# Kernel tuning notes

Hardware: AMD Instinct MI355X
Metric: run time of the kernel (lower is better)

## Reference

```python
import jax, jax.numpy as jnp
import numpy as np

N_NODES = 50000
N_EDGES = 800000
IN_C, HID_C, OUT_C = 256, 256, 128


def setup_inputs() -> dict:
    key = jax.random.key(0)
    k1, k2, k3, k4 = jax.random.split(key, 4)
    x = jax.random.normal(k1, (N_NODES, IN_C), dtype=jnp.float32)
    edge_index = jax.random.randint(k2, (2, N_EDGES), 0, N_NODES, dtype=jnp.int64)
    # Glorot-ish init for linear weights, zero bias (PyG GCNConv default)
    W1 = jax.random.normal(k3, (IN_C, HID_C), dtype=jnp.float32) / np.sqrt(IN_C)
    b1 = jnp.zeros((HID_C,), dtype=jnp.float32)
    W2 = jax.random.normal(k4, (HID_C, OUT_C), dtype=jnp.float32) / np.sqrt(HID_C)
    b2 = jnp.zeros((OUT_C,), dtype=jnp.float32)
    return {"x": x, "edge_index": edge_index, "W1": W1, "b1": b1, "W2": W2, "b2": b2}


def _gcn_conv(x, src, dst, norm, W, b):
    # Linear transform first (dense GEMM), then normalized scatter-add aggregation.
    h = x @ W                                   # [N, out]
    msg = h[src] * norm[:, None]                # [E+N, out] gathered, scaled messages
    out = jax.ops.segment_sum(msg, dst, num_segments=x.shape[0])
    return out + b


def reference(x, edge_index, W1, b1, W2, b2):
    n = x.shape[0]
    loops = jnp.arange(n, dtype=edge_index.dtype)
    # PyG GCNConv: add self-loops, symmetric normalization D^-1/2 A D^-1/2
    src = jnp.concatenate([edge_index[0], loops])
    dst = jnp.concatenate([edge_index[1], loops])
    deg = jnp.zeros((n,), dtype=x.dtype).at[dst].add(1.0)
    dinv = jnp.where(deg > 0, jax.lax.rsqrt(deg), 0.0)
    norm = dinv[src] * dinv[dst]                # [E+N]
    h = jax.nn.relu(_gcn_conv(x, src, dst, norm, W1, b1))
    return _gcn_conv(h, src, dst, norm, W2, b2)
```

## Files before the change

kernel.cpp:

```cpp
#include <hip/hip_runtime.h>


#define NN 50000
#define EE 800000
#define IN_C 256
#define HID_C 256
#define OUT_C 128
#define CAP 64
#define FILLB 2048

typedef __attribute__((ext_vector_type(8))) short short8;
typedef __attribute__((ext_vector_type(4))) float f32x4;
typedef __attribute__((ext_vector_type(2))) float f32x2;

static __device__ __forceinline__ ushort f2b(float f) {
    union { float f; unsigned u; } v; v.f = f;
    unsigned r = v.u + 0x7FFF + ((v.u >> 16) & 1);
    return (ushort)(r >> 16);
}


__global__ __launch_bounds__(256) void build_kernel(
    const int* __restrict__ src, const int* __restrict__ dst,
    int* __restrict__ cnt, ushort* __restrict__ slots,
    ushort* __restrict__ hb, ushort* __restrict__ h2b, int e) {
    const int bid = blockIdx.x;
    const int tid = threadIdx.x;
    if (bid < FILLB) {
        const int xcd = bid & 7;
        const int lo = xcd * (NN / 8);
        const int hi = lo + (NN / 8);
        const int sub = bid >> 3;
        for (int i = sub * 256 + tid; i < e; i += 256 * 256) {
            int d = dst[i];
            if (d >= lo && d < hi) {
                int s = src[i];
                int pos = atomicAdd(&cnt[d], 1);
                if (pos < CAP) slots[(size_t)d * CAP + pos] = (ushort)s;
            }
        }
    } else {
        ushort4 z = {0, 0, 0, 0};
        if (tid < 64) ((ushort4*)(hb + (size_t)NN * HID_C))[tid] = z;
        else if (tid < 96) ((ushort4*)(h2b + (size_t)NN * OUT_C))[tid - 64] = z;
    }
}


template <bool A_FP32, int NHALF>
__global__ __launch_bounds__(256) void gemm_kernel(
    const void* __restrict__ Av, const float* __restrict__ W,
    const int* __restrict__ cnt, ushort* __restrict__ C, int M, int Ntot) {
    constexpr int KK = 256;
    __shared__ ushort wt[128 * KK];

    const int tid = threadIdx.x;
    const int rowBase = blockIdx.x * 128;

    const int wave = tid >> 6, lane = tid & 63;
    const int l15 = lane & 15, lk = lane >> 4;

    int r0 = rowBase + wave * 32 + l15;
    int ra0 = min(r0, M - 1);
    int ra1 = min(r0 + 16, M - 1);

    short8 a0f[8], a1f[8];
    if constexpr (A_FP32) {
        const float* A = (const float*)Av;
        const float* Ar0 = A + (size_t)ra0 * KK + lk * 8;
        const float* Ar1 = A + (size_t)ra1 * KK + lk * 8;
#pragma unroll
        for (int ks = 0; ks < 8; ++ks) {
            float4 p0 = *(const float4*)(Ar0 + ks * 32);
            float4 p1 = *(const float4*)(Ar0 + ks * 32 + 4);
            float4 q0 = *(const float4*)(Ar1 + ks * 32);
            float4 q1 = *(const float4*)(Ar1 + ks * 32 + 4);
            short8 a, b;
            a[0] = f2b(p0.x); a[1] = f2b(p0.y); a[2] = f2b(p0.z); a[3] = f2b(p0.w);
            a[4] = f2b(p1.x); a[5] = f2b(p1.y); a[6] = f2b(p1.z); a[7] = f2b(p1.w);
            b[0] = f2b(q0.x); b[1] = f2b(q0.y); b[2] = f2b(q0.z); b[3] = f2b(q0.w);
            b[4] = f2b(q1.x); b[5] = f2b(q1.y); b[6] = f2b(q1.z); b[7] = f2b(q1.w);
            a0f[ks] = a; a1f[ks] = b;
        }
    } else {
        const ushort* A = (const ushort*)Av;
        const ushort* Ar0 = A + (size_t)ra0 * KK + lk * 8;
        const ushort* Ar1 = A + (size_t)ra1 * KK + lk * 8;
#pragma unroll
        for (int ks = 0; ks < 8; ++ks) {
            a0f[ks] = *(const short8*)(Ar0 + ks * 32);
            a1f[ks] = *(const short8*)(Ar1 + ks * 32);
        }
    }

    for (int hh = 0; hh < NHALF; ++hh) {
        const int colBase = hh * 128;
        for (int it = 0; it < 32; ++it) {
            int item = tid + it * 256;
            int n = item & 127;
            int kg = item >> 7;
            int k = kg * 4;
            const float* wp = W + (size_t)k * Ntot + colBase + n;
            ushort4 o;
            o.x = f2b(wp[0]);
            o.y = f2b(wp[Ntot]);
            o.z = f2b(wp[2 * Ntot]);
            o.w = f2b(wp[3 * Ntot]);
            *(ushort4*)((char*)wt + n * 512 + ((kg * 8) ^ ((n & 7) << 4))) = o;
        }
        __syncthreads();

        f32x4 acc[2][8] = {};
#pragma unroll
        for (int ks = 0; ks < 8; ++ks) {
            int kbyte = ks * 64 + lk * 16;
#pragma unroll
            for (int nt = 0; nt < 8; ++nt) {
                int n = nt * 16 + l15;
                short8 b = *(const short8*)((const char*)wt + n * 512 + (kbyte ^ ((n & 7) << 4)));
                acc[0][nt] = __builtin_amdgcn_mfma_f32_16x16x32_bf16(a0f[ks], b, acc[0][nt], 0, 0, 0);
                acc[1][nt] = __builtin_amdgcn_mfma_f32_16x16x32_bf16(a1f[ks], b, acc[1][nt], 0, 0, 0);
            }
        }

#pragma unroll
        for (int t = 0; t < 2; ++t) {
            int rbase = rowBase + wave * 32 + t * 16 + lk * 4;
#pragma unroll
            for (int r = 0; r < 4; ++r) {
                int row = rbase + r;
                if (row < M) {
                    float dv = rsqrtf((float)(cnt[row] + 1));
#pragma unroll
                    for (int nt = 0; nt < 8; ++nt)
                        C[(size_t)row * Ntot + colBase + nt * 16 + l15] = f2b(acc[t][nt][r] * dv);
                }
            }
        }
        if (hh + 1 < NHALF) __syncthreads();
    }
}


template <int C, bool RELU, bool OUT_BF16>
__global__ __launch_bounds__(256) void gather_kernel(
    const ushort* __restrict__ h, const int* __restrict__ cnt,
    const ushort* __restrict__ slots, const float* __restrict__ bias,
    void* __restrict__ out, int n) {
    constexpr int VPL = C / 64;
    const int node = blockIdx.x * 4 + (threadIdx.x >> 6);
    if (node >= n) return;
    const int lane = threadIdx.x & 63;
    const int c0 = cnt[node];
    const int deg = min(c0, CAP);
    const ushort* sl = slots + (size_t)node * CAP;
    const ushort* hl = h + lane * VPL;

    f32x2 acc01 = {0.f, 0.f}, acc23 = {0.f, 0.f};

    auto addu = [&](unsigned u, f32x2& acc) {
        f32x2 p;
        p.x = __uint_as_float(u << 16);
        p.y = __uint_as_float(u & 0xFFFF0000u);
        acc += p;
    };

    for (int base = 0; base < deg; base += 16) {
        uint4 pa = *(const uint4*)(sl + base);
        uint4 pb = *(const uint4*)(sl + base + 8);
        int id[16];
        id[0]  = pa.x & 0xFFFF; id[1]  = pa.x >> 16;
        id[2]  = pa.y & 0xFFFF; id[3]  = pa.y >> 16;
        id[4]  = pa.z & 0xFFFF; id[5]  = pa.z >> 16;
        id[6]  = pa.w & 0xFFFF; id[7]  = pa.w >> 16;
        id[8]  = pb.x & 0xFFFF; id[9]  = pb.x >> 16;
        id[10] = pb.y & 0xFFFF; id[11] = pb.y >> 16;
        id[12] = pb.z & 0xFFFF; id[13] = pb.z >> 16;
        id[14] = pb.w & 0xFFFF; id[15] = pb.w >> 16;
        int ix[16];
#pragma unroll
        for (int j = 0; j < 16; ++j) ix[j] = (base + j < deg) ? id[j] : n;
        if constexpr (VPL == 4) {
            uint2 v[16];
#pragma unroll
            for (int j = 0; j < 16; ++j) v[j] = *(const uint2*)(hl + (size_t)ix[j] * C);
#pragma unroll
            for (int j = 0; j < 16; ++j) { addu(v[j].x, acc01); addu(v[j].y, acc23); }
        } else {
            unsigned v[16];
#pragma unroll
            for (int j = 0; j < 16; ++j) v[j] = *(const unsigned*)(hl + (size_t)ix[j] * C);
#pragma unroll
            for (int j = 0; j < 16; ++j) addu(v[j], acc01);
        }
    }

    if constexpr (VPL == 4) {
        uint2 v = *(const uint2*)(hl + (size_t)node * C);
        addu(v.x, acc01); addu(v.y, acc23);
    } else {
        unsigned v = *(const unsigned*)(hl + (size_t)node * C);
        addu(v, acc01);
    }

    const float dv = rsqrtf((float)(c0 + 1));
    const float* bp = bias + lane * VPL;
    float r[VPL];
    r[0] = acc01.x * dv + bp[0];
    r[1] = acc01.y * dv + bp[1];
    if constexpr (VPL == 4) {
        r[2] = acc23.x * dv + bp[2];
        r[3] = acc23.y * dv + bp[3];
    }
#pragma unroll
    for (int k = 0; k < VPL; ++k)
        if (RELU) r[k] = fmaxf(r[k], 0.0f);

    if constexpr (OUT_BF16) {
        ushort* op = (ushort*)out + (size_t)node * C + lane * VPL;
#pragma unroll
        for (int k = 0; k < VPL; ++k) op[k] = f2b(r[k]);
    } else {
        float* op = (float*)out + (size_t)node * C + lane * VPL;
#pragma unroll
        for (int k = 0; k < VPL; ++k) op[k] = r[k];
    }
}


extern "C" void kernel_launch(void* const* d_in, const int* in_sizes, int n_in,
                              void* d_out, int out_size, void* d_ws, size_t ws_size,
                              hipStream_t stream) {
    const float* x  = (const float*)d_in[0];
    const int*   ei = (const int*)d_in[1];
    const float* W1 = (const float*)d_in[2];
    const float* b1 = (const float*)d_in[3];
    const float* W2 = (const float*)d_in[4];
    const float* b2 = (const float*)d_in[5];
    float* out = (float*)d_out;

    const int N = in_sizes[0] / IN_C;
    const int E = in_sizes[1] / 2;
    const int* src = ei;
    const int* dst = ei + E;

    char* ws = (char*)d_ws;
    int*    cnt   = (int*)(ws + (256 << 10));
    ushort* slots = (ushort*)(ws + (512 << 10));
    ushort* hb    = (ushort*)(ws + (size_t)(40 << 20));
    ushort* h1b   = (ushort*)(ws + (size_t)(66 << 20));
    ushort* h2b   = (ushort*)(ws + (size_t)(92 << 20));

    hipMemsetAsync(cnt, 0, (size_t)N * sizeof(int), stream);
    build_kernel<<<FILLB + 1, 256, 0, stream>>>(src, dst, cnt, slots, hb, h2b, E);

    gemm_kernel<true, 2><<<(N + 127) / 128, 256, 0, stream>>>(x, W1, cnt, hb, N, HID_C);
    gather_kernel<HID_C, true, true><<<(N + 3) / 4, 256, 0, stream>>>(
        hb, cnt, slots, b1, h1b, N);

    gemm_kernel<false, 1><<<(N + 127) / 128, 256, 0, stream>>>(h1b, W2, cnt, h2b, N, OUT_C);
    gather_kernel<OUT_C, false, false><<<(N + 3) / 4, 256, 0, stream>>>(
        h2b, cnt, slots, b2, out, N);
}
```

Measured before the change: 183.8 us.

## Fuse first GEMM with CSR build and weight layer-1 gather by source dinv

Merges the adjacency-building kernel and the first GEMM into one launch, so the GEMM blocks run alongside the atomic slot fill instead of waiting for it. Because the GEMM no longer knows the degrees, the source-side normalisation moves into the layer-1 gather as a per-neighbour dinv weight, and a small dinv kernel precomputes rsqrt degrees. Counters are split into two halves per node to reduce atomic contention. The cost is an extra launch, an extra dinv gather per neighbour in layer 1, and two segment loops per node.

New measurement: 248.9 us. 1.35x slower.

```diff
diff --git a/kernel.cpp b/kernel.cpp
--- a/kernel.cpp
+++ b/kernel.cpp
@@ -7,7 +7,9 @@
 #define HID_C 256
 #define OUT_C 128
 #define CAP 64
+#define SEGC 32
 #define FILLB 2048
+#define G1B 391
 
 typedef __attribute__((ext_vector_type(8))) short short8;
 typedef __attribute__((ext_vector_type(4))) float f32x4;
@@ -20,43 +22,43 @@
 }
 
 
-__global__ __launch_bounds__(256) void build_kernel(
+__global__ __launch_bounds__(256) void fused1_kernel(
+    const float* __restrict__ x, const float* __restrict__ W1,
     const int* __restrict__ src, const int* __restrict__ dst,
     int* __restrict__ cnt, ushort* __restrict__ slots,
-    ushort* __restrict__ hb, ushort* __restrict__ h2b, int e) {
+    ushort* __restrict__ hb, ushort* __restrict__ h2b, int e, int M) {
     const int bid = blockIdx.x;
     const int tid = threadIdx.x;
-    if (bid < FILLB) {
-        const int xcd = bid & 7;
-        const int lo = xcd * (NN / 8);
-        const int hi = lo + (NN / 8);
-        const int sub = bid >> 3;
-        for (int i = sub * 256 + tid; i < e; i += 256 * 256) {
-            int d = dst[i];
-            if (d >= lo && d < hi) {
-                int s = src[i];
-                int pos = atomicAdd(&cnt[d], 1);
-                if (pos < CAP) slots[(size_t)d * CAP + pos] = (ushort)s;
-            }
-        }
-    } else {
-        ushort4 z = {0, 0, 0, 0};
-        if (tid < 64) ((ushort4*)(hb + (size_t)NN * HID_C))[tid] = z;
-        else if (tid < 96) ((ushort4*)(h2b + (size_t)NN * OUT_C))[tid - 64] = z;
-    }
-}
-
-
-template <bool A_FP32, int NHALF>
-__global__ __launch_bounds__(256) void gemm_kernel(
-    const void* __restrict__ Av, const float* __restrict__ W,
-    const int* __restrict__ cnt, ushort* __restrict__ C, int M, int Ntot) {
+
+    if (bid >= G1B) {
+        if (bid < G1B + FILLB) {
+            const int fb = bid - G1B;
+            const int xcd = fb & 7;
+            const int lo = xcd * (NN / 8);
+            const int hi = lo + (NN / 8);
+            const int sub = fb >> 3;
+            const int half = sub >> 7;
+            for (int i = sub * 256 + tid; i < e; i += 256 * 256) {
+                int d = dst[i];
+                if (d >= lo && d < hi) {
+                    int s = src[i];
+                    int pos = atomicAdd(&cnt[2 * d + half], 1);
+                    if (pos < SEGC)
+                        slots[(size_t)d * CAP + half * SEGC + pos] = (ushort)s;
+                }
+            }
+        } else {
+            ushort4 z = {0, 0, 0, 0};
+            if (tid < 64) ((ushort4*)(hb + (size_t)NN * HID_C))[tid] = z;
+            else if (tid < 96) ((ushort4*)(h2b + (size_t)NN * OUT_C))[tid - 64] = z;
+        }
+        return;
+    }
+
     constexpr int KK = 256;
     __shared__ ushort wt[128 * KK];
 
-    const int tid = threadIdx.x;
-    const int rowBase = blockIdx.x * 128;
-
+    const int rowBase = bid * 128;
     const int wave = tid >> 6, lane = tid & 63;
     const int l15 = lane & 15, lk = lane >> 4;
 
@@ -65,10 +67,9 @@
     int ra1 = min(r0 + 16, M - 1);
 
     short8 a0f[8], a1f[8];
-    if constexpr (A_FP32) {
-        const float* A = (const float*)Av;
-        const float* Ar0 = A + (size_t)ra0 * KK + lk * 8;
-        const float* Ar1 = A + (size_t)ra1 * KK + lk * 8;
+    {
+        const float* Ar0 = x + (size_t)ra0 * KK + lk * 8;
+        const float* Ar1 = x + (size_t)ra1 * KK + lk * 8;
 #pragma unroll
         for (int ks = 0; ks < 8; ++ks) {
             float4 p0 = *(const float4*)(Ar0 + ks * 32);
@@ -82,30 +83,21 @@
             b[4] = f2b(q1.x); b[5] = f2b(q1.y); b[6] = f2b(q1.z); b[7] = f2b(q1.w);
             a0f[ks] = a; a1f[ks] = b;
         }
-    } else {
-        const ushort* A = (const ushort*)Av;
-        const ushort* Ar0 = A + (size_t)ra0 * KK + lk * 8;
-        const ushort* Ar1 = A + (size_t)ra1 * KK + lk * 8;
-#pragma unroll
-        for (int ks = 0; ks < 8; ++ks) {
-            a0f[ks] = *(const short8*)(Ar0 + ks * 32);
-            a1f[ks] = *(const short8*)(Ar1 + ks * 32);
-        }
-    }
-
-    for (int hh = 0; hh < NHALF; ++hh) {
+    }
+
+    for (int hh = 0; hh < 2; ++hh) {
         const int colBase = hh * 128;
         for (int it = 0; it < 32; ++it) {
             int item = tid + it * 256;
             int n = item & 127;
             int kg = item >> 7;
             int k = kg * 4;
-            const float* wp = W + (size_t)k * Ntot + colBase + n;
+            const float* wp = W1 + (size_t)k * HID_C + colBase + n;
             ushort4 o;
             o.x = f2b(wp[0]);
-            o.y = f2b(wp[Ntot]);
-            o.z = f2b(wp[2 * Ntot]);
-            o.w = f2b(wp[3 * Ntot]);
+            o.y = f2b(wp[HID_C]);
+            o.z = f2b(wp[2 * HID_C]);
+            o.w = f2b(wp[3 * HID_C]);
             *(ushort4*)((char*)wt + n * 512 + ((kg * 8) ^ ((n & 7) << 4))) = o;
         }
         __syncthreads();
@@ -130,80 +122,163 @@
             for (int r = 0; r < 4; ++r) {
                 int row = rbase + r;
                 if (row < M) {
-                    float dv = rsqrtf((float)(cnt[row] + 1));
 #pragma unroll
                     for (int nt = 0; nt < 8; ++nt)
-                        C[(size_t)row * Ntot + colBase + nt * 16 + l15] = f2b(acc[t][nt][r] * dv);
+                        hb[(size_t)row * HID_C + colBase + nt * 16 + l15] = f2b(acc[t][nt][r]);
                 }
             }
         }
-        if (hh + 1 < NHALF) __syncthreads();
-    }
-}
-
-
-template <int C, bool RELU, bool OUT_BF16>
+        if (hh == 0) __syncthreads();
+    }
+}
+
+
+__global__ void dinv_kernel(const int* __restrict__ cnt, float* __restrict__ dinv, int n) {
+    int i = blockIdx.x * blockDim.x + threadIdx.x;
+    if (i < n) dinv[i] = rsqrtf((float)(cnt[2 * i] + cnt[2 * i + 1] + 1));
+    else if (i == n) dinv[i] = 0.0f;
+}
+
+
+__global__ __launch_bounds__(256) void gemm2_kernel(
+    const ushort* __restrict__ A, const float* __restrict__ W,
+    const float* __restrict__ dinv, ushort* __restrict__ C, int M) {
+    constexpr int KK = 256;
+    __shared__ ushort wt[128 * KK];
+
+    const int tid = threadIdx.x;
+    const int rowBase = blockIdx.x * 128;
+    const int wave = tid >> 6, lane = tid & 63;
+    const int l15 = lane & 15, lk = lane >> 4;
+
+    for (int it = 0; it < 32; ++it) {
+        int item = tid + it * 256;
+        int n = item & 127;
+        int kg = item >> 7;
+        int k = kg * 4;
+        const float* wp = W + (size_t)k * OUT_C + n;
+        ushort4 o;
+        o.x = f2b(wp[0]);
+        o.y = f2b(wp[OUT_C]);
+        o.z = f2b(wp[2 * OUT_C]);
+        o.w = f2b(wp[3 * OUT_C]);
+        *(ushort4*)((char*)wt + n * 512 + ((kg * 8) ^ ((n & 7) << 4))) = o;
+    }
+    __syncthreads();
+
+    int r0 = rowBase + wave * 32 + l15;
+    int ra0 = min(r0, M - 1);
+    int ra1 = min(r0 + 16, M - 1);
+    const ushort* Ar0 = A + (size_t)ra0 * KK + lk * 8;
+    const ushort* Ar1 = A + (size_t)ra1 * KK + lk * 8;
+
+    f32x4 acc[2][8] = {};
+#pragma unroll
+    for (int ks = 0; ks < 8; ++ks) {
+        short8 a0 = *(const short8*)(Ar0 + ks * 32);
+        short8 a1 = *(const short8*)(Ar1 + ks * 32);
+        int kbyte = ks * 64 + lk * 16;
+#pragma unroll
+        for (int nt = 0; nt < 8; ++nt) {
+            int n = nt * 16 + l15;
+            short8 b = *(const short8*)((const char*)wt + n * 512 + (kbyte ^ ((n & 7) << 4)));
+            acc[0][nt] = __builtin_amdgcn_mfma_f32_16x16x32_bf16(a0, b, acc[0][nt], 0, 0, 0);
+            acc[1][nt] = __builtin_amdgcn_mfma_f32_16x16x32_bf16(a1, b, acc[1][nt], 0, 0, 0);
+        }
+    }
+
+#pragma unroll
+    for (int t = 0; t < 2; ++t) {
+        int rbase = rowBase + wave * 32 + t * 16 + lk * 4;
+#pragma unroll
+        for (int r = 0; r < 4; ++r) {
+            int row = rbase + r;
+            if (row < M) {
+                float dv = dinv[row];
+#pragma unroll
+                for (int nt = 0; nt < 8; ++nt)
+                    C[(size_t)row * OUT_C + nt * 16 + l15] = f2b(acc[t][nt][r] * dv);
+            }
+        }
+    }
+}
+
+
+template <int C, bool RELU, bool OUT_BF16, bool WEIGHTED>
 __global__ __launch_bounds__(256) void gather_kernel(
     const ushort* __restrict__ h, const int* __restrict__ cnt,
-    const ushort* __restrict__ slots, const float* __restrict__ bias,
-    void* __restrict__ out, int n) {
+    const ushort* __restrict__ slots, const float* __restrict__ dinv,
+    const float* __restrict__ bias, void* __restrict__ out, int n) {
     constexpr int VPL = C / 64;
     const int node = blockIdx.x * 4 + (threadIdx.x >> 6);
     if (node >= n) return;
     const int lane = threadIdx.x & 63;
-    const int c0 = cnt[node];
-    const int deg = min(c0, CAP);
+    const int2 cs = *(const int2*)(cnt + 2 * node);
     const ushort* sl = slots + (size_t)node * CAP;
     const ushort* hl = h + lane * VPL;
 
     f32x2 acc01 = {0.f, 0.f}, acc23 = {0.f, 0.f};
 
-    auto addu = [&](unsigned u, f32x2& acc) {
+    auto addu = [&](unsigned u, float w, f32x2& acc) {
         f32x2 p;
         p.x = __uint_as_float(u << 16);
         p.y = __uint_as_float(u & 0xFFFF0000u);
-        acc += p;
+        if (WEIGHTED) { f32x2 ww = {w, w}; acc += p * ww; }
+        else acc += p;
     };
 
-    for (int base = 0; base < deg; base += 16) {
-        uint4 pa = *(const uint4*)(sl + base);
-        uint4 pb = *(const uint4*)(sl + base + 8);
-        int id[16];
-        id[0]  = pa.x & 0xFFFF; id[1]  = pa.x >> 16;
-        id[2]  = pa.y & 0xFFFF; id[3]  = pa.y >> 16;
-        id[4]  = pa.z & 0xFFFF; id[5]  = pa.z >> 16;
-        id[6]  = pa.w & 0xFFFF; id[7]  = pa.w >> 16;
-        id[8]  = pb.x & 0xFFFF; id[9]  = pb.x >> 16;
-        id[10] = pb.y & 0xFFFF; id[11] = pb.y >> 16;
-        id[12] = pb.z & 0xFFFF; id[13] = pb.z >> 16;
-        id[14] = pb.w & 0xFFFF; id[15] = pb.w >> 16;
-        int ix[16];
-#pragma unroll
-        for (int j = 0; j < 16; ++j) ix[j] = (base + j < deg) ? id[j] : n;
-        if constexpr (VPL == 4) {
-            uint2 v[16];
-#pragma unroll
-            for (int j = 0; j < 16; ++j) v[j] = *(const uint2*)(hl + (size_t)ix[j] * C);
-#pragma unroll
-            for (int j = 0; j < 16; ++j) { addu(v[j].x, acc01); addu(v[j].y, acc23); }
-        } else {
-            unsigned v[16];
-#pragma unroll
-            for (int j = 0; j < 16; ++j) v[j] = *(const unsigned*)(hl + (size_t)ix[j] * C);
-#pragma unroll
-            for (int j = 0; j < 16; ++j) addu(v[j], acc01);
-        }
-    }
-
+#pragma unroll
+    for (int seg = 0; seg < 2; ++seg) {
+        const int degS = min(seg ? cs.y : cs.x, SEGC);
+        const ushort* sls = sl + seg * SEGC;
+        for (int base = 0; base < degS; base += 16) {
+            uint4 pa = *(const uint4*)(sls + base);
+            uint4 pb = *(const uint4*)(sls + base + 8);
+            int id[16];
+            id[0]  = pa.x & 0xFFFF; id[1]  = pa.x >> 16;
+            id[2]  = pa.y & 0xFFFF; id[3]  = pa.y >> 16;
+            id[4]  = pa.z & 0xFFFF; id[5]  = pa.z >> 16;
+            id[6]  = pa.w & 0xFFFF; id[7]  = pa.w >> 16;
+            id[8]  = pb.x & 0xFFFF; id[9]  = pb.x >> 16;
+            id[10] = pb.y & 0xFFFF; id[11] = pb.y >> 16;
+            id[12] = pb.z & 0xFFFF; id[13] = pb.z >> 16;
+            id[14] = pb.w & 0xFFFF; id[15] = pb.w >> 16;
+            int ix[16];
+#pragma unroll
+            for (int j = 0; j < 16; ++j) ix[j] = (base + j < degS) ? id[j] : n;
+            float w[16];
+            if (WEIGHTED) {
+#pragma unroll
+                for (int j = 0; j < 16; ++j) w[j] = dinv[ix[j]];
+            }
+            if constexpr (VPL == 4) {
+                uint2 v[16];
+#pragma unroll
+                for (int j = 0; j < 16; ++j) v[j] = *(const uint2*)(hl + (size_t)ix[j] * C);
+#pragma unroll
+                for (int j = 0; j < 16; ++j) {
+                    addu(v[j].x, WEIGHTED ? w[j] : 0.f, acc01);
+                    addu(v[j].y, WEIGHTED ? w[j] : 0.f, acc23);
+                }
+            } else {
+                unsigned v[16];
+#pragma unroll
+                for (int j = 0; j < 16; ++j) v[j] = *(const unsigned*)(hl + (size_t)ix[j] * C);
+#pragma unroll
+                for (int j = 0; j < 16; ++j) addu(v[j], WEIGHTED ? w[j] : 0.f, acc01);
+            }
+        }
+    }
+
+    const float dv = dinv[node];
     if constexpr (VPL == 4) {
         uint2 v = *(const uint2*)(hl + (size_t)node * C);
-        addu(v.x, acc01); addu(v.y, acc23);
+        addu(v.x, dv, acc01); addu(v.y, dv, acc23);
     } else {
         unsigned v = *(const unsigned*)(hl + (size_t)node * C);
-        addu(v, acc01);
-    }
-
-    const float dv = rsqrtf((float)(c0 + 1));
+        addu(v, dv, acc01);
+    }
+
     const float* bp = bias + lane * VPL;
     float r[VPL];
     r[0] = acc01.x * dv + bp[0];
@@ -245,20 +320,22 @@
     const int* dst = ei + E;
 
     char* ws = (char*)d_ws;
+    float*  dinv  = (float*)(ws);
     int*    cnt   = (int*)(ws + (256 << 10));
-    ushort* slots = (ushort*)(ws + (512 << 10));
+    ushort* slots = (ushort*)(ws + (768 << 10));
     ushort* hb    = (ushort*)(ws + (size_t)(40 << 20));
     ushort* h1b   = (ushort*)(ws + (size_t)(66 << 20));
     ushort* h2b   = (ushort*)(ws + (size_t)(92 << 20));
 
-    hipMemsetAsync(cnt, 0, (size_t)N * sizeof(int), stream);
-    build_kernel<<<FILLB + 1, 256, 0, stream>>>(src, dst, cnt, slots, hb, h2b, E);
-
-    gemm_kernel<true, 2><<<(N + 127) / 128, 256, 0, stream>>>(x, W1, cnt, hb, N, HID_C);
-    gather_kernel<HID_C, true, true><<<(N + 3) / 4, 256, 0, stream>>>(
-        hb, cnt, slots, b1, h1b, N);
-
-    gemm_kernel<false, 1><<<(N + 127) / 128, 256, 0, stream>>>(h1b, W2, cnt, h2b, N, OUT_C);
-    gather_kernel<OUT_C, false, false><<<(N + 3) / 4, 256, 0, stream>>>(
-        h2b, cnt, slots, b2, out, N);
-}
+    hipMemsetAsync(cnt, 0, (size_t)2 * N * sizeof(int), stream);
+    fused1_kernel<<<G1B + FILLB + 1, 256, 0, stream>>>(
+        x, W1, src, dst, cnt, slots, hb, h2b, E, N);
+    dinv_kernel<<<(N + 256) / 256, 256, 0, stream>>>(cnt, dinv, N);
+
+    gather_kernel<HID_C, true, true, true><<<(N + 3) / 4, 256, 0, stream>>>(
+        hb, cnt, slots, dinv, b1, h1b, N);
+
+    gemm2_kernel<<<(N + 127) / 128, 256, 0, stream>>>(h1b, W2, dinv, h2b, N);
+    gather_kernel<OUT_C, false, false, false><<<(N + 3) / 4, 256, 0, stream>>>(
+        h2b, cnt, slots, dinv, b2, out, N);
+}
```

## Split gather aggregation into channel slices across blocks for cache locality

Applied to the files above, without the earlier changes.

Restructures the neighbor-aggregation kernel so each block handles 16 nodes but only a 32-channel slice (64 bytes) of the feature row. Consecutive blocks cover the different slices of the same node group, so the neighbor rows they gather overlap in time. Each 16-lane group now does 4-byte loads instead of 64 lanes doing 8-byte loads per node. The aim is to improve L2/MALL reuse and raise the number of memory requests in flight. In exchange, the slot lists and counts are read several times and each gather access becomes narrower, 64-byte segments per row.

Result: slower. 208.4 us (+13.4%).

```diff
diff --git a/kernel.cpp b/kernel.cpp
--- a/kernel.cpp
+++ b/kernel.cpp
@@ -142,23 +142,28 @@
 }
 
 
-template <int C, bool RELU, bool OUT_BF16>
-__global__ __launch_bounds__(256) void gather_kernel(
+template <int C, int NSLICE, bool RELU, bool OUT_BF16>
+__global__ __launch_bounds__(256) void gatherS_kernel(
     const ushort* __restrict__ h, const int* __restrict__ cnt,
     const ushort* __restrict__ slots, const float* __restrict__ bias,
     void* __restrict__ out, int n) {
-    constexpr int VPL = C / 64;
-    const int node = blockIdx.x * 4 + (threadIdx.x >> 6);
+    constexpr int SH = (NSLICE == 8) ? 3 : 2;
+    const int bid = blockIdx.x;
+    const int slice = bid & (NSLICE - 1);
+    const int g = bid >> SH;
+    const int tid = threadIdx.x;
+    const int node = g * 16 + (tid >> 4);
     if (node >= n) return;
-    const int lane = threadIdx.x & 63;
+    const int l16 = tid & 15;
+    const int ch = slice * 32 + l16 * 2;
+
     const int c0 = cnt[node];
     const int deg = min(c0, CAP);
     const ushort* sl = slots + (size_t)node * CAP;
-    const ushort* hl = h + lane * VPL;
-
-    f32x2 acc01 = {0.f, 0.f}, acc23 = {0.f, 0.f};
-
-    auto addu = [&](unsigned u, f32x2& acc) {
+    const ushort* hc = h + ch;
+
+    f32x2 acc = {0.f, 0.f};
+    auto addu = [&](unsigned u) {
         f32x2 p;
         p.x = __uint_as_float(u << 16);
         p.y = __uint_as_float(u & 0xFFFF0000u);
@@ -180,50 +185,27 @@
         int ix[16];
 #pragma unroll
         for (int j = 0; j < 16; ++j) ix[j] = (base + j < deg) ? id[j] : n;
-        if constexpr (VPL == 4) {
-            uint2 v[16];
-#pragma unroll
-            for (int j = 0; j < 16; ++j) v[j] = *(const uint2*)(hl + (size_t)ix[j] * C);
-#pragma unroll
-            for (int j = 0; j < 16; ++j) { addu(v[j].x, acc01); addu(v[j].y, acc23); }
-        } else {
-            unsigned v[16];
-#pragma unroll
-            for (int j = 0; j < 16; ++j) v[j] = *(const unsigned*)(hl + (size_t)ix[j] * C);
-#pragma unroll
-            for (int j = 0; j < 16; ++j) addu(v[j], acc01);
-        }
-    }
-
-    if constexpr (VPL == 4) {
-        uint2 v = *(const uint2*)(hl + (size_t)node * C);
-        addu(v.x, acc01); addu(v.y, acc23);
+        unsigned v[16];
+#pragma unroll
+        for (int j = 0; j < 16; ++j) v[j] = *(const unsigned*)(hc + (size_t)ix[j] * C);
+#pragma unroll
+        for (int j = 0; j < 16; ++j) addu(v[j]);
+    }
+
+    addu(*(const unsigned*)(hc + (size_t)node * C));
+
+    const float dv = rsqrtf((float)(c0 + 1));
+    const float* bp = bias + ch;
+    float r0 = acc.x * dv + bp[0];
+    float r1 = acc.y * dv + bp[1];
+    if (RELU) { r0 = fmaxf(r0, 0.0f); r1 = fmaxf(r1, 0.0f); }
+
+    if constexpr (OUT_BF16) {
+        ushort2 o; o.x = f2b(r0); o.y = f2b(r1);
+        *(ushort2*)((ushort*)out + (size_t)node * C + ch) = o;
     } else {
-        unsigned v = *(const unsigned*)(hl + (size_t)node * C);
-        addu(v, acc01);
-    }
-
-    const float dv = rsqrtf((float)(c0 + 1));
-    const float* bp = bias + lane * VPL;
-    float r[VPL];
-    r[0] = acc01.x * dv + bp[0];
-    r[1] = acc01.y * dv + bp[1];
-    if constexpr (VPL == 4) {
-        r[2] = acc23.x * dv + bp[2];
-        r[3] = acc23.y * dv + bp[3];
-    }
-#pragma unroll
-    for (int k = 0; k < VPL; ++k)
-        if (RELU) r[k] = fmaxf(r[k], 0.0f);
-
-    if constexpr (OUT_BF16) {
-        ushort* op = (ushort*)out + (size_t)node * C + lane * VPL;
-#pragma unroll
-        for (int k = 0; k < VPL; ++k) op[k] = f2b(r[k]);
-    } else {
-        float* op = (float*)out + (size_t)node * C + lane * VPL;
-#pragma unroll
-        for (int k = 0; k < VPL; ++k) op[k] = r[k];
+        float2 o; o.x = r0; o.y = r1;
+        *(float2*)((float*)out + (size_t)node * C + ch) = o;
     }
 }
 
@@ -251,14 +233,16 @@
     ushort* h1b   = (ushort*)(ws + (size_t)(66 << 20));
     ushort* h2b   = (ushort*)(ws + (size_t)(92 << 20));
 
+    const int ngroups = (N + 15) / 16;
+
     hipMemsetAsync(cnt, 0, (size_t)N * sizeof(int), stream);
     build_kernel<<<FILLB + 1, 256, 0, stream>>>(src, dst, cnt, slots, hb, h2b, E);
 
     gemm_kernel<true, 2><<<(N + 127) / 128, 256, 0, stream>>>(x, W1, cnt, hb, N, HID_C);
-    gather_kernel<HID_C, true, true><<<(N + 3) / 4, 256, 0, stream>>>(
+    gatherS_kernel<HID_C, 8, true, true><<<ngroups * 8, 256, 0, stream>>>(
         hb, cnt, slots, b1, h1b, N);
 
     gemm_kernel<false, 1><<<(N + 127) / 128, 256, 0, stream>>>(h1b, W2, cnt, h2b, N, OUT_C);
-    gather_kernel<OUT_C, false, false><<<(N + 3) / 4, 256, 0, stream>>>(
+    gatherS_kernel<OUT_C, 4, false, false><<<ngroups * 4, 256, 0, stream>>>(
         h2b, cnt, slots, b2, out, N);
 }
```

## Process several nodes per wave in gather with prefetched slot lists

Applied to the files above, without the earlier changes.

The gather kernel now has each wave handle K=8 consecutive nodes instead of one. It prefetches the next node's degree and first 32 neighbour slots while the current node is being aggregated. The first 32 neighbours are also gathered in one batch of 16 or 32 loads, with a loop only for any extra neighbours. This aims to hide the latency of the count and slot loads and to keep more gathers in flight. In exchange it raises register pressure and cuts the grid by 8x, which may lower parallelism and occupancy.

Result: slower. 191.8 us (+4.4%).

```diff
diff --git a/kernel.cpp b/kernel.cpp
--- a/kernel.cpp
+++ b/kernel.cpp
@@ -142,88 +142,184 @@
 }
 
 
-template <int C, bool RELU, bool OUT_BF16>
+template <int C, bool RELU, bool OUT_BF16, int K>
 __global__ __launch_bounds__(256) void gather_kernel(
     const ushort* __restrict__ h, const int* __restrict__ cnt,
     const ushort* __restrict__ slots, const float* __restrict__ bias,
     void* __restrict__ out, int n) {
     constexpr int VPL = C / 64;
-    const int node = blockIdx.x * 4 + (threadIdx.x >> 6);
-    if (node >= n) return;
+    const int wid = blockIdx.x * 4 + (threadIdx.x >> 6);
     const int lane = threadIdx.x & 63;
-    const int c0 = cnt[node];
-    const int deg = min(c0, CAP);
-    const ushort* sl = slots + (size_t)node * CAP;
+    int nd = wid * K;
+    if (nd >= n) return;
     const ushort* hl = h + lane * VPL;
-
-    f32x2 acc01 = {0.f, 0.f}, acc23 = {0.f, 0.f};
-
-    auto addu = [&](unsigned u, f32x2& acc) {
-        f32x2 p;
-        p.x = __uint_as_float(u << 16);
-        p.y = __uint_as_float(u & 0xFFFF0000u);
-        acc += p;
-    };
-
-    for (int base = 0; base < deg; base += 16) {
-        uint4 pa = *(const uint4*)(sl + base);
-        uint4 pb = *(const uint4*)(sl + base + 8);
-        int id[16];
-        id[0]  = pa.x & 0xFFFF; id[1]  = pa.x >> 16;
-        id[2]  = pa.y & 0xFFFF; id[3]  = pa.y >> 16;
-        id[4]  = pa.z & 0xFFFF; id[5]  = pa.z >> 16;
-        id[6]  = pa.w & 0xFFFF; id[7]  = pa.w >> 16;
-        id[8]  = pb.x & 0xFFFF; id[9]  = pb.x >> 16;
-        id[10] = pb.y & 0xFFFF; id[11] = pb.y >> 16;
-        id[12] = pb.z & 0xFFFF; id[13] = pb.z >> 16;
-        id[14] = pb.w & 0xFFFF; id[15] = pb.w >> 16;
-        int ix[16];
-#pragma unroll
-        for (int j = 0; j < 16; ++j) ix[j] = (base + j < deg) ? id[j] : n;
+    const float* bp = bias + lane * VPL;
+
+    int c0 = cnt[nd];
+    const ushort* sl0 = slots + (size_t)nd * CAP;
+    uint4 s0 = *(const uint4*)(sl0);
+    uint4 s1 = *(const uint4*)(sl0 + 8);
+    uint4 s2 = *(const uint4*)(sl0 + 16);
+    uint4 s3 = *(const uint4*)(sl0 + 24);
+
+    for (int k = 0; k < K && nd < n; ++k) {
+        const int ndN = nd + 1;
+        const bool hasN = (k + 1 < K) && (ndN < n);
+        int cN = 0;
+        uint4 t0 = {}, t1 = {}, t2 = {}, t3 = {};
+        if (hasN) {
+            const ushort* slN = slots + (size_t)ndN * CAP;
+            cN = cnt[ndN];
+            t0 = *(const uint4*)(slN);
+            t1 = *(const uint4*)(slN + 8);
+            t2 = *(const uint4*)(slN + 16);
+            t3 = *(const uint4*)(slN + 24);
+        }
+
+        const int deg = min(c0, CAP);
+        int id[32];
+        id[0]  = s0.x & 0xFFFF; id[1]  = s0.x >> 16;
+        id[2]  = s0.y & 0xFFFF; id[3]  = s0.y >> 16;
+        id[4]  = s0.z & 0xFFFF; id[5]  = s0.z >> 16;
+        id[6]  = s0.w & 0xFFFF; id[7]  = s0.w >> 16;
+        id[8]  = s1.x & 0xFFFF; id[9]  = s1.x >> 16;
+        id[10] = s1.y & 0xFFFF; id[11] = s1.y >> 16;
+        id[12] = s1.z & 0xFFFF; id[13] = s1.z >> 16;
+        id[14] = s1.w & 0xFFFF; id[15] = s1.w >> 16;
+        id[16] = s2.x & 0xFFFF; id[17] = s2.x >> 16;
+        id[18] = s2.y & 0xFFFF; id[19] = s2.y >> 16;
+        id[20] = s2.z & 0xFFFF; id[21] = s2.z >> 16;
+        id[22] = s2.w & 0xFFFF; id[23] = s2.w >> 16;
+        id[24] = s3.x & 0xFFFF; id[25] = s3.x >> 16;
+        id[26] = s3.y & 0xFFFF; id[27] = s3.y >> 16;
+        id[28] = s3.z & 0xFFFF; id[29] = s3.z >> 16;
+        id[30] = s3.w & 0xFFFF; id[31] = s3.w >> 16;
+
+        f32x2 acc01 = {0.f, 0.f}, acc23 = {0.f, 0.f};
+        auto addu = [&](unsigned u, f32x2& acc) {
+            f32x2 p;
+            p.x = __uint_as_float(u << 16);
+            p.y = __uint_as_float(u & 0xFFFF0000u);
+            acc += p;
+        };
+
         if constexpr (VPL == 4) {
-            uint2 v[16];
-#pragma unroll
-            for (int j = 0; j < 16; ++j) v[j] = *(const uint2*)(hl + (size_t)ix[j] * C);
-#pragma unroll
-            for (int j = 0; j < 16; ++j) { addu(v[j].x, acc01); addu(v[j].y, acc23); }
+            uint2 vself = *(const uint2*)(hl + (size_t)nd * C);
+
+            if (deg <= 16) {
+                int ix[16];
+#pragma unroll
+                for (int j = 0; j < 16; ++j) ix[j] = (j < deg) ? id[j] : n;
+                uint2 v[16];
+#pragma unroll
+                for (int j = 0; j < 16; ++j) v[j] = *(const uint2*)(hl + (size_t)ix[j] * C);
+#pragma unroll
+                for (int j = 0; j < 16; ++j) { addu(v[j].x, acc01); addu(v[j].y, acc23); }
+            } else {
+                int ix[32];
+#pragma unroll
+                for (int j = 0; j < 32; ++j) ix[j] = (j < deg) ? id[j] : n;
+                uint2 v[32];
+#pragma unroll
+                for (int j = 0; j < 32; ++j) v[j] = *(const uint2*)(hl + (size_t)ix[j] * C);
+#pragma unroll
+                for (int j = 0; j < 32; ++j) { addu(v[j].x, acc01); addu(v[j].y, acc23); }
+            }
+            const ushort* sl = slots + (size_t)nd * CAP;
+            for (int base = 32; base < deg; base += 16) {
+                uint4 pa = *(const uint4*)(sl + base);
+                uint4 pb = *(const uint4*)(sl + base + 8);
+                int jd[16];
+                jd[0]  = pa.x & 0xFFFF; jd[1]  = pa.x >> 16;
+                jd[2]  = pa.y & 0xFFFF; jd[3]  = pa.y >> 16;
+                jd[4]  = pa.z & 0xFFFF; jd[5]  = pa.z >> 16;
+                jd[6]  = pa.w & 0xFFFF; jd[7]  = pa.w >> 16;
+                jd[8]  = pb.x & 0xFFFF; jd[9]  = pb.x >> 16;
+                jd[10] = pb.y & 0xFFFF; jd[11] = pb.y >> 16;
+                jd[12] = pb.z & 0xFFFF; jd[13] = pb.z >> 16;
+                jd[14] = pb.w & 0xFFFF; jd[15] = pb.w >> 16;
+                int jx[16];
+#pragma unroll
+                for (int j = 0; j < 16; ++j) jx[j] = (base + j < deg) ? jd[j] : n;
+                uint2 v[16];
+#pragma unroll
+                for (int j = 0; j < 16; ++j) v[j] = *(const uint2*)(hl + (size_t)jx[j] * C);
+#pragma unroll
+                for (int j = 0; j < 16; ++j) { addu(v[j].x, acc01); addu(v[j].y, acc23); }
+            }
+            addu(vself.x, acc01); addu(vself.y, acc23);
         } else {
-            unsigned v[16];
-#pragma unroll
-            for (int j = 0; j < 16; ++j) v[j] = *(const unsigned*)(hl + (size_t)ix[j] * C);
-#pragma unroll
-            for (int j = 0; j < 16; ++j) addu(v[j], acc01);
-        }
-    }
-
-    if constexpr (VPL == 4) {
-        uint2 v = *(const uint2*)(hl + (size_t)node * C);
-        addu(v.x, acc01); addu(v.y, acc23);
-    } else {
-        unsigned v = *(const unsigned*)(hl + (size_t)node * C);
-        addu(v, acc01);
-    }
-
-    const float dv = rsqrtf((float)(c0 + 1));
-    const float* bp = bias + lane * VPL;
-    float r[VPL];
-    r[0] = acc01.x * dv + bp[0];
-    r[1] = acc01.y * dv + bp[1];
-    if constexpr (VPL == 4) {
-        r[2] = acc23.x * dv + bp[2];
-        r[3] = acc23.y * dv + bp[3];
-    }
-#pragma unroll
-    for (int k = 0; k < VPL; ++k)
-        if (RELU) r[k] = fmaxf(r[k], 0.0f);
-
-    if constexpr (OUT_BF16) {
-        ushort* op = (ushort*)out + (size_t)node * C + lane * VPL;
-#pragma unroll
-        for (int k = 0; k < VPL; ++k) op[k] = f2b(r[k]);
-    } else {
-        float* op = (float*)out + (size_t)node * C + lane * VPL;
-#pragma unroll
-        for (int k = 0; k < VPL; ++k) op[k] = r[k];
+            unsigned vself = *(const unsigned*)(hl + (size_t)nd * C);
+
+            if (deg <= 16) {
+                int ix[16];
+#pragma unroll
+                for (int j = 0; j < 16; ++j) ix[j] = (j < deg) ? id[j] : n;
+                unsigned v[16];
+#pragma unroll
+                for (int j = 0; j < 16; ++j) v[j] = *(const unsigned*)(hl + (size_t)ix[j] * C);
+#pragma unroll
+                for (int j = 0; j < 16; ++j) addu(v[j], acc01);
+            } else {
+                int ix[32];
+#pragma unroll
+                for (int j = 0; j < 32; ++j) ix[j] = (j < deg) ? id[j] : n;
+                unsigned v[32];
+#pragma unroll
+                for (int j = 0; j < 32; ++j) v[j] = *(const unsigned*)(hl + (size_t)ix[j] * C);
+#pragma unroll
+                for (int j = 0; j < 32; ++j) addu(v[j], acc01);
+            }
+            const ushort* sl = slots + (size_t)nd * CAP;
+            for (int base = 32; base < deg; base += 16) {
+                uint4 pa = *(const uint4*)(sl + base);
+                uint4 pb = *(const uint4*)(sl + base + 8);
+                int jd[16];
+                jd[0]  = pa.x & 0xFFFF; jd[1]  = pa.x >> 16;
+                jd[2]  = pa.y & 0xFFFF; jd[3]  = pa.y >> 16;
+                jd[4]  = pa.z & 0xFFFF; jd[5]  = pa.z >> 16;
+                jd[6]  = pa.w & 0xFFFF; jd[7]  = pa.w >> 16;
+                jd[8]  = pb.x & 0xFFFF; jd[9]  = pb.x >> 16;
+                jd[10] = pb.y & 0xFFFF; jd[11] = pb.y >> 16;
+                jd[12] = pb.z & 0xFFFF; jd[13] = pb.z >> 16;
+                jd[14] = pb.w & 0xFFFF; jd[15] = pb.w >> 16;
+                int jx[16];
+#pragma unroll
+                for (int j = 0; j < 16; ++j) jx[j] = (base + j < deg) ? jd[j] : n;
+                unsigned v[16];
+#pragma unroll
+                for (int j = 0; j < 16; ++j) v[j] = *(const unsigned*)(hl + (size_t)jx[j] * C);
+#pragma unroll
+                for (int j = 0; j < 16; ++j) addu(v[j], acc01);
+            }
+            addu(vself, acc01);
+        }
+
+        const float dv = rsqrtf((float)(c0 + 1));
+        float r[VPL];
+        r[0] = acc01.x * dv + bp[0];
+        r[1] = acc01.y * dv + bp[1];
+        if constexpr (VPL == 4) {
+            r[2] = acc23.x * dv + bp[2];
+            r[3] = acc23.y * dv + bp[3];
+        }
+#pragma unroll
+        for (int q = 0; q < VPL; ++q)
+            if (RELU) r[q] = fmaxf(r[q], 0.0f);
+
+        if constexpr (OUT_BF16) {
+            ushort* op = (ushort*)out + (size_t)nd * C + lane * VPL;
+#pragma unroll
+            for (int q = 0; q < VPL; ++q) op[q] = f2b(r[q]);
+        } else {
+            float* op = (float*)out + (size_t)nd * C + lane * VPL;
+#pragma unroll
+            for (int q = 0; q < VPL; ++q) op[q] = r[q];
+        }
+
+        nd = ndN;
+        c0 = cN;
+        s0 = t0; s1 = t1; s2 = t2; s3 = t3;
     }
 }
 
@@ -251,14 +347,17 @@
     ushort* h1b   = (ushort*)(ws + (size_t)(66 << 20));
     ushort* h2b   = (ushort*)(ws + (size_t)(92 << 20));
 
+    constexpr int K = 8;
+    const int gblocks = (N + 4 * K - 1) / (4 * K);
+
     hipMemsetAsync(cnt, 0, (size_t)N * sizeof(int), stream);
     build_kernel<<<FILLB + 1, 256, 0, stream>>>(src, dst, cnt, slots, hb, h2b, E);
 
     gemm_kernel<true, 2><<<(N + 127) / 128, 256, 0, stream>>>(x, W1, cnt, hb, N, HID_C);
-    gather_kernel<HID_C, true, true><<<(N + 3) / 4, 256, 0, stream>>>(
+    gather_kernel<HID_C, true, true, K><<<gblocks, 256, 0, stream>>>(
         hb, cnt, slots, b1, h1b, N);
 
     gemm_kernel<false, 1><<<(N + 127) / 128, 256, 0, stream>>>(h1b, W2, cnt, h2b, N, OUT_C);
-    gather_kernel<OUT_C, false, false><<<(N + 3) / 4, 256, 0, stream>>>(
+    gather_kernel<OUT_C, false, false, K><<<gblocks, 256, 0, stream>>>(
         h2b, cnt, slots, b2, out, N);
 }
```
